# Performance work log

Hardware: AMD Instinct MI355X
Metric: run time of the kernel (lower is better)

## Reference

```python
import jax, jax.numpy as jnp
import numpy as np

GRID = 385  # (W+1) = (H+1) = (D+1) corners of a 384^3 voxel grid


def setup_inputs() -> dict:
    key = jax.random.key(0)
    occ = jax.random.uniform(key, (GRID, GRID, GRID), dtype=jnp.float32)
    return {"occ": occ}


def reference(occ):
    # Occupancy connectivity loss: sum over axis-aligned neighbor pairs of
    # |occ_i - occ_j| (each pair counted once via the 3 forward directions).
    lx = jnp.sum(jnp.abs(occ[1:, :, :] - occ[:-1, :, :]))
    ly = jnp.sum(jnp.abs(occ[:, 1:, :] - occ[:, :-1, :]))
    lz = jnp.sum(jnp.abs(occ[:, :, 1:] - occ[:, :, :-1]))
    return lx + ly + lz
```

## Files before the change

### kernel.cpp

```cpp
#include <hip/hip_runtime.h>


constexpr int G     = 385;
constexpr int PLANE = G * G;

#define TPB   256
#define ZT    3
#define YT    12
#define XC    16
#define XP    24
#define NBLK  (ZT * YT * XC)
#define S     140

typedef float f4v __attribute__((ext_vector_type(4)));

static __device__ __forceinline__ f4v ldg4u(const float* __restrict__ p) {
    f4v r;
    __builtin_memcpy(&r, p, sizeof(r));
    return r;
}

__global__ __launch_bounds__(TPB) void occ_conn_main(
    const float* __restrict__ a, float* __restrict__ ws)
{
    __shared__ float T[2][33][S];
    float s = 0.f;

    const int tz = threadIdx.x & 31;
    const int ty = threadIdx.x >> 5;

    int t = blockIdx.x;
    const int bc = t % XC;  t /= XC;
    const int by = t % YT;  t /= YT;
    const int bz = t;
    const unsigned gy0 = by * 32u;
    const unsigned gz0 = bz * 128u;
    const int  P0    = bc * XP;
    const bool lastc = (bc == XC - 1);
    const bool ey    = (by == YT - 1);
    const bool ez    = (bz == ZT - 1);

    f4v m0, m1, m2, m3;
    f4v p0, p1, p2, p3;
    f4v q0, q1, q2, q3;
    f4v h, hp, hq;
    float h2 = 0.f, h2p = 0.f, h2q = 0.f;

    const float* rowp = a + ((unsigned)P0 * (unsigned)PLANE + gy0 * (unsigned)G + gz0);

    for (int tt = 0; tt <= XP + 1; ++tt) {
        if (tt <= XP) {
            const float* rp = rowp + 4u * (unsigned)tz;
            m0 = ldg4u(rp + (unsigned)(ty     ) * G);
            m1 = ldg4u(rp + (unsigned)(ty +  8) * G);
            m2 = ldg4u(rp + (unsigned)(ty + 16) * G);
            m3 = ldg4u(rp + (unsigned)(ty + 24) * G);
            if (ty == 0) {
                h = ldg4u(rowp + 32u * G + 4u * (unsigned)tz);
            } else if (ty == 1) {
                h[0] = rowp[(unsigned)tz * G + 128u];
            } else if (ty == 2 && tz == 0) {
                h2 = rowp[32u * G + 128u];
            }
        }

        if (tt >= 1) {
            const int xc = tt - 1;
            const float (*C)[S] = T[(tt - 1) & 1];
            const bool zy = (xc < XP) || (lastc && xc == XP);
            const bool xd = (tt >= 2);

            if (zy) {
                #pragma unroll
                for (int rr = 0; rr < 4; ++rr) {
                    const int r = ty + 8 * rr;
                    const f4v v = rr == 0 ? p0 : rr == 1 ? p1 : rr == 2 ? p2 : p3;
                    s += fabsf(v[1] - v[0]) + fabsf(v[2] - v[1]) + fabsf(v[3] - v[2]);
                    float zb = __shfl_down(v[0], 1);
                    if (tz == 31) zb = C[r][128];
                    s += fabsf(zb - v[3]);
                    const f4v yn = *(const f4v*)&C[r + 1][4 * tz];
                    s += fabsf(yn[0] - v[0]) + fabsf(yn[1] - v[1])
                       + fabsf(yn[2] - v[2]) + fabsf(yn[3] - v[3]);
                }
                if (ey && ty == 0) {
                    s += fabsf(hp[1] - hp[0]) + fabsf(hp[2] - hp[1]) + fabsf(hp[3] - hp[2]);
                    float zb = __shfl_down(hp[0], 1);
                    if (tz == 31) zb = C[32][128];
                    s += fabsf(zb - hp[3]);
                }
                if (ez && ty == 1) {
                    s += fabsf(C[tz + 1][128] - hp[0]);
                }
            }

            if (xd) {
                #pragma unroll
                for (int rr = 0; rr < 4; ++rr) {
                    const f4v v = rr == 0 ? p0 : rr == 1 ? p1 : rr == 2 ? p2 : p3;
                    const f4v w = rr == 0 ? q0 : rr == 1 ? q1 : rr == 2 ? q2 : q3;
                    s += fabsf(w[0] - v[0]) + fabsf(w[1] - v[1])
                       + fabsf(w[2] - v[2]) + fabsf(w[3] - v[3]);
                }
                if (ey && ty == 0)
                    s += fabsf(hp[0] - hq[0]) + fabsf(hp[1] - hq[1])
                       + fabsf(hp[2] - hq[2]) + fabsf(hp[3] - hq[3]);
                if (ez && ty == 1)                        s += fabsf(hp[0] - hq[0]);
                if (ey && ez && ty == 2 && tz == 0)       s += fabsf(h2p - h2q);
            }
        }

        if (tt <= XP) {
            float (*B)[S] = T[tt & 1];
            *(f4v*)&B[ty      ][4 * tz] = m0;
            *(f4v*)&B[ty +  8][4 * tz] = m1;
            *(f4v*)&B[ty + 16][4 * tz] = m2;
            *(f4v*)&B[ty + 24][4 * tz] = m3;
            if      (ty == 0)            *(f4v*)&B[32][4 * tz] = h;
            else if (ty == 1)            B[tz][128] = h[0];
            else if (ty == 2 && tz == 0) B[32][128] = h2;
            q0 = p0; q1 = p1; q2 = p2; q3 = p3;
            p0 = m0; p1 = m1; p2 = m2; p3 = m3;
            hq = hp; hp = h;  h2q = h2p; h2p = h2;
            rowp += PLANE;
        }
        __syncthreads();
    }

    #pragma unroll
    for (int off = 32; off > 0; off >>= 1) s += __shfl_down(s, off, 64);
    __shared__ float ls[TPB / 64];
    const int lane = threadIdx.x & 63;
    const int wid  = threadIdx.x >> 6;
    if (lane == 0) ls[wid] = s;
    __syncthreads();
    if (threadIdx.x == 0) {
        float tsum = 0.f;
        #pragma unroll
        for (int w = 0; w < TPB / 64; ++w) tsum += ls[w];
        ws[blockIdx.x] = tsum;
    }
}

__global__ __launch_bounds__(256) void occ_conn_final(
    const float* __restrict__ ws, float* __restrict__ out)
{
    float s = 0.f;
    for (int i = threadIdx.x; i < NBLK; i += 256) s += ws[i];
    #pragma unroll
    for (int off = 32; off > 0; off >>= 1) s += __shfl_down(s, off, 64);
    __shared__ float ls[4];
    const int lane = threadIdx.x & 63;
    const int wid  = threadIdx.x >> 6;
    if (lane == 0) ls[wid] = s;
    __syncthreads();
    if (threadIdx.x == 0) out[0] = ls[0] + ls[1] + ls[2] + ls[3];
}

extern "C" void kernel_launch(void* const* d_in, const int* in_sizes, int n_in,
                              void* d_out, int out_size, void* d_ws, size_t ws_size,
                              hipStream_t stream)
{
    const float* a   = (const float*)d_in[0];
    float*       out = (float*)d_out;
    float*       ws  = (float*)d_ws;

    occ_conn_main<<<NBLK, TPB, 0, stream>>>(a, ws);
    occ_conn_final<<<1, 256, 0, stream>>>(ws, out);
}
```

Before: 315.8 us.

## Deepen register prefetch pipeline so global loads land two iterations ahead

Adds an extra stage of register buffers (n0..n3, hn, h2n) so each plane's global loads are issued one iteration earlier than their shared-memory store, and compute runs two iterations behind the load. The aim is to hide global memory latency behind a full iteration of compute instead of having to wait for the loads before the same iteration's LDS store. In exchange it uses more VGPRs, which may lower occupancy, and adds one more loop iteration per block.

```diff
diff --git a/kernel.cpp b/kernel.cpp
--- a/kernel.cpp
+++ b/kernel.cpp
@@ -41,14 +41,15 @@
     const bool ez    = (bz == ZT - 1);
 
     f4v m0, m1, m2, m3;
+    f4v n0, n1, n2, n3;
     f4v p0, p1, p2, p3;
     f4v q0, q1, q2, q3;
-    f4v h, hp, hq;
-    float h2 = 0.f, h2p = 0.f, h2q = 0.f;
+    f4v h, hn, hp, hq;
+    float h2 = 0.f, h2n = 0.f, h2p = 0.f, h2q = 0.f;
 
     const float* rowp = a + ((unsigned)P0 * (unsigned)PLANE + gy0 * (unsigned)G + gz0);
 
-    for (int tt = 0; tt <= XP + 1; ++tt) {
+    for (int tt = 0; tt <= XP + 2; ++tt) {
         if (tt <= XP) {
             const float* rp = rowp + 4u * (unsigned)tz;
             m0 = ldg4u(rp + (unsigned)(ty     ) * G);
@@ -64,11 +65,11 @@
             }
         }
 
-        if (tt >= 1) {
-            const int xc = tt - 1;
-            const float (*C)[S] = T[(tt - 1) & 1];
+        if (tt >= 2) {
+            const int xc = tt - 2;
+            const float (*C)[S] = T[xc & 1];
             const bool zy = (xc < XP) || (lastc && xc == XP);
-            const bool xd = (tt >= 2);
+            const bool xd = (xc >= 1);
 
             if (zy) {
                 #pragma unroll
@@ -110,18 +111,25 @@
             }
         }
 
+        if (tt >= 1 && tt <= XP + 1) {
+            float (*B)[S] = T[(tt - 1) & 1];
+            *(f4v*)&B[ty      ][4 * tz] = n0;
+            *(f4v*)&B[ty +  8][4 * tz] = n1;
+            *(f4v*)&B[ty + 16][4 * tz] = n2;
+            *(f4v*)&B[ty + 24][4 * tz] = n3;
+            if      (ty == 0)            *(f4v*)&B[32][4 * tz] = hn;
+            else if (ty == 1)            B[tz][128] = hn[0];
+            else if (ty == 2 && tz == 0) B[32][128] = h2n;
+        }
+
+        if (tt <= XP + 1) {
+            q0 = p0; q1 = p1; q2 = p2; q3 = p3;
+            p0 = n0; p1 = n1; p2 = n2; p3 = n3;
+            hq = hp; hp = hn; h2q = h2p; h2p = h2n;
+        }
         if (tt <= XP) {
-            float (*B)[S] = T[tt & 1];
-            *(f4v*)&B[ty      ][4 * tz] = m0;
-            *(f4v*)&B[ty +  8][4 * tz] = m1;
-            *(f4v*)&B[ty + 16][4 * tz] = m2;
-            *(f4v*)&B[ty + 24][4 * tz] = m3;
-            if      (ty == 0)            *(f4v*)&B[32][4 * tz] = h;
-            else if (ty == 1)            B[tz][128] = h[0];
-            else if (ty == 2 && tz == 0) B[32][128] = h2;
-            q0 = p0; q1 = p1; q2 = p2; q3 = p3;
-            p0 = m0; p1 = m1; p2 = m2; p3 = m3;
-            hq = hp; hp = h;  h2q = h2p; h2p = h2;
+            n0 = m0; n1 = m1; n2 = m2; n3 = m3;
+            hn = h;  h2n = h2;
             rowp += PLANE;
         }
         __syncthreads();
```

Result: no change. 315.2 us (-0.2%).
